# Kernel tuning notes

Hardware: AMD Instinct MI355X
Metric: run time of the kernel (lower is better)

Reference implementation:

```python
import jax, jax.numpy as jnp
import numpy as np

GROUPS = 32
NUM_HEADS = 8
EPS = 1e-5


def setup_inputs() -> dict:
    key = jax.random.key(0)
    ks = jax.random.split(key, 8)
    b, c, h, w = 2, 256, 64, 64
    x = jax.random.normal(ks[0], (b, c, h, w), dtype=jnp.float32)
    gn_w = jnp.ones((c,), dtype=jnp.float32)
    gn_b = jnp.zeros((c,), dtype=jnp.float32)
    qkv_w = jax.random.normal(ks[1], (3 * c, c), dtype=jnp.float32) * 0.02  # 1x1 conv
    qkv_b = jnp.zeros((3 * c,), dtype=jnp.float32)
    proj_w = jax.random.normal(ks[2], (c, c), dtype=jnp.float32) * 0.02  # 1x1 conv
    proj_b = jnp.zeros((c,), dtype=jnp.float32)
    return {"x": x, "gn_w": gn_w, "gn_b": gn_b, "qkv_w": qkv_w,
            "qkv_b": qkv_b, "proj_w": proj_w, "proj_b": proj_b}


def _group_norm(x, w, b):
    bsz, c, h, wd = x.shape
    xg = x.reshape(bsz, GROUPS, c // GROUPS, h * wd)
    mean = jnp.mean(xg, axis=(2, 3), keepdims=True)
    var = jnp.mean(jnp.square(xg - mean), axis=(2, 3), keepdims=True)
    xn = ((xg - mean) * jax.lax.rsqrt(var + EPS)).reshape(bsz, c, h, wd)
    return xn * w[None, :, None, None] + b[None, :, None, None]


def reference(x, gn_w, gn_b, qkv_w, qkv_b, proj_w, proj_b):
    b, c, h, w = x.shape
    hd = c // NUM_HEADS
    s = h * w
    xn = _group_norm(x, gn_w, gn_b)
    # 1x1 conv == channel matmul
    qkv = jnp.einsum('oc,bcs->bos', qkv_w, xn.reshape(b, c, s)) + qkv_b[None, :, None]
    qkv = qkv.reshape(b, 3, NUM_HEADS, hd, s)
    q, k, v = qkv[:, 0], qkv[:, 1], qkv[:, 2]  # (b, nh, hd, s)
    scale = 1.0 / jnp.sqrt(jnp.asarray(hd, dtype=x.dtype))
    scores = jnp.einsum('bhds,bhdt->bhst', q, k) * scale  # (b, nh, s, s)
    attn = jax.nn.softmax(scores, axis=-1)
    out = jnp.einsum('bhst,bhdt->bhds', attn, v)  # (b, nh, hd, s)
    out = out.reshape(b, c, h, w)
    out = jnp.einsum('oc,bcs->bos', proj_w, out.reshape(b, c, s)).reshape(b, c, h, w)
    out = out + proj_b[None, :, None, None]
    return out + x
```

## Files before the change

### kernel.cpp

```cpp
#include <hip/hip_runtime.h>
#include <hip/hip_bf16.h>

#define B_ 2
#define C_ 256
#define S_ 4096
#define NH 8
#define HD 32
#define EPSV 1e-5f
#define QSC2 0.25503487942324256f

typedef __bf16 bf16_t;
typedef bf16_t bf16x8 __attribute__((ext_vector_type(8)));
typedef float f32x4 __attribute__((ext_vector_type(4)));
typedef float f32x16 __attribute__((ext_vector_type(16)));
typedef int i32x2 __attribute__((ext_vector_type(2)));
typedef __hip_bfloat16 hbf;

__device__ inline unsigned cvtpk_bf16(float a, float b) {
  unsigned r;
  asm("v_cvt_pk_bf16_f32 %0, %1, %2" : "=v"(r) : "v"(a), "v"(b));
  return r;
}

#if __has_builtin(__builtin_amdgcn_exp2f)
#define EXP2R(x) __builtin_amdgcn_exp2f(x)
#else
#define EXP2R(x) exp2f(x)
#endif

__global__ __launch_bounds__(256) void f2bf_kernel(const float* __restrict__ src, hbf* __restrict__ dst, int n) {
  int i = blockIdx.x * 256 + threadIdx.x;
  if (i < n) dst[i] = __float2bfloat16(src[i]);
}

__global__ __launch_bounds__(256) void wfrag_kernel(const float* __restrict__ src, hbf* __restrict__ dst, int nchunks) {
  int i = blockIdx.x * 256 + threadIdx.x;
  if (i >= nchunks) return;
  int o = i >> 5, c8 = (i & 31) * 8;
  alignas(16) hbf tmp[8];
#pragma unroll
  for (int j = 0; j < 8; j++) tmp[j] = __float2bfloat16(src[(size_t)o * C_ + c8 + j]);
  *(uint4*)&dst[(((size_t)(o >> 5) * 16) + (c8 >> 4)) * 512 + (o & 31) * 16 + (c8 & 15)] = *(uint4*)tmp;
}

__global__ __launch_bounds__(1024) void gn_kernel(const float* __restrict__ x, const float* __restrict__ gw,
                                                  const float* __restrict__ gb, hbf* __restrict__ xn) {
  int b = blockIdx.x >> 5, g = blockIdx.x & 31;
  const float* xp = x + ((size_t)b * C_ + g * 8) * S_;
  float sum = 0.f, sumsq = 0.f;
  const float4* xp4 = (const float4*)xp;
  for (int i = threadIdx.x; i < 8 * S_ / 4; i += 1024) {
    float4 v = xp4[i];
    sum += v.x + v.y + v.z + v.w;
    sumsq += v.x * v.x + v.y * v.y + v.z * v.z + v.w * v.w;
  }
#pragma unroll
  for (int off = 32; off > 0; off >>= 1) {
    sum += __shfl_down(sum, off);
    sumsq += __shfl_down(sumsq, off);
  }
  __shared__ float red[2][16];
  int wid = threadIdx.x >> 6;
  if ((threadIdx.x & 63) == 0) { red[0][wid] = sum; red[1][wid] = sumsq; }
  __syncthreads();
  sum = 0.f; sumsq = 0.f;
#pragma unroll
  for (int k = 0; k < 16; k++) { sum += red[0][k]; sumsq += red[1][k]; }
  const float inv_n = 1.f / (8 * S_);
  float mean = sum * inv_n;
  float rstd = rsqrtf(fmaxf(sumsq * inv_n - mean * mean, 0.f) + EPSV);
  float scv[8], shv[8];
#pragma unroll
  for (int c = 0; c < 8; c++) {
    scv[c] = gw[g * 8 + c] * rstd;
    shv[c] = gb[g * 8 + c] - mean * scv[c];
  }
  for (int s = threadIdx.x; s < S_; s += 1024) {
    alignas(16) hbf tmp[8];
#pragma unroll
    for (int c = 0; c < 8; c++)
      tmp[c] = __float2bfloat16(xp[(size_t)c * S_ + s] * scv[c] + shv[c]);
    *(uint4*)&xn[(((size_t)b * (S_ >> 5) + (s >> 5)) * 16 + (g >> 1)) * 512 + (s & 31) * 16 + (g & 1) * 8] =
        *(uint4*)tmp;
  }
}

__global__ __launch_bounds__(512, 4) void qkv_gemm(const hbf* __restrict__ xn, const hbf* __restrict__ wf,
                                                   const float* __restrict__ bias,
                                                   hbf* __restrict__ qbuf, hbf* __restrict__ kg,
                                                   hbf* __restrict__ vg) {
  int bt = blockIdx.z;
  int m0 = blockIdx.x * 128;
  int n0 = blockIdx.y * 128;
  int tid = threadIdx.x, lane = tid & 63, w = tid >> 6;
  int wq = w & 3, wo = w >> 2;
  int l31 = lane & 31, hi = lane >> 5;
  const int loff = l31 * 16 + hi * 8;
  const hbf* ap = xn + ((size_t)bt * (S_ >> 5) + (m0 >> 5) + wq) * 8192;
  int oc0 = n0 + wo * 64;
  const hbf* bp0 = wf + (size_t)(oc0 >> 5) * 8192;
  const hbf* bp1 = bp0 + 8192;
  f32x16 acc0 = {0.f,0.f,0.f,0.f,0.f,0.f,0.f,0.f,0.f,0.f,0.f,0.f,0.f,0.f,0.f,0.f};
  f32x16 acc1 = acc0;
#pragma unroll 4
  for (int ks = 0; ks < 16; ++ks) {
    bf16x8 af = *(const bf16x8*)(ap + ks * 512 + loff);
    bf16x8 b0 = *(const bf16x8*)(bp0 + ks * 512 + loff);
    bf16x8 b1 = *(const bf16x8*)(bp1 + ks * 512 + loff);
    acc0 = __builtin_amdgcn_mfma_f32_32x32x16_bf16(af, b0, acc0, 0, 0, 0);
    acc1 = __builtin_amdgcn_mfma_f32_32x32x16_bf16(af, b1, acc1, 0, 0, 0);
  }
  int s_base = m0 + wq * 32;
#pragma unroll
  for (int ct = 0; ct < 2; ++ct) {
    f32x16 a = ct ? acc1 : acc0;
    int oc = oc0 + ct * 32;
    int o = oc + l31;
    float bs = bias[o];
    if (oc < 256) {
#pragma unroll
      for (int r = 0; r < 16; r++) {
        int s = s_base + (r & 3) + 8 * (r >> 2) + 4 * hi;
        qbuf[((size_t)bt * S_ + s) * C_ + o] = __float2bfloat16((a[r] + bs) * QSC2);
      }
    } else if (oc < 512) {
      int hh = (oc - 256) >> 5;
      const size_t khead = (size_t)(bt * NH + hh) * (S_ >> 5);
#pragma unroll
      for (int r = 0; r < 16; r++) {
        int s = s_base + (r & 3) + 8 * (r >> 2) + 4 * hi;
        kg[(khead + (s >> 5)) * 1024 + (l31 >> 4) * 512 + (s & 31) * 16 + (l31 & 15)] =
            __float2bfloat16(a[r] + bs);
      }
    } else {
      int hh = (oc - 512) >> 5;
      const size_t vhead = (size_t)(bt * NH + hh) * (S_ >> 4);
#pragma unroll
      for (int r = 0; r < 16; r++) {
        int s = s_base + (r & 3) + 8 * (r >> 2) + 4 * hi;
        vg[(vhead + (s >> 4)) * 512 + l31 * 16 + (s & 15)] = __float2bfloat16(a[r] + bs);
      }
    }
  }
}

__device__ inline void softmax_pv(f32x16 sc, bf16x8 va0, bf16x8 va1,
                                  f32x16& o_acc, float& l_run) {
#pragma unroll
  for (int i = 0; i < 16; i++) sc[i] = EXP2R(sc[i]);
  {
    float s0a = sc[0] + sc[1], s1a = sc[2] + sc[3], s2a = sc[4] + sc[5], s3a = sc[6] + sc[7];
    float s4a = sc[8] + sc[9], s5a = sc[10] + sc[11], s6a = sc[12] + sc[13], s7a = sc[14] + sc[15];
    s0a += s1a; s2a += s3a; s4a += s5a; s6a += s7a;
    s0a += s2a; s4a += s6a;
    l_run += s0a + s4a;
  }
#pragma unroll
  for (int kb = 0; kb < 2; kb++) {
    unsigned a0 = cvtpk_bf16(sc[kb * 8 + 0], sc[kb * 8 + 1]);
    unsigned b0 = cvtpk_bf16(sc[kb * 8 + 2], sc[kb * 8 + 3]);
    unsigned a1 = cvtpk_bf16(sc[kb * 8 + 4], sc[kb * 8 + 5]);
    unsigned b1 = cvtpk_bf16(sc[kb * 8 + 6], sc[kb * 8 + 7]);
    i32x2 ra = __builtin_amdgcn_permlane32_swap((int)a0, (int)a1, false, false);
    i32x2 rb = __builtin_amdgcn_permlane32_swap((int)b0, (int)b1, false, false);
    union { unsigned u[4]; bf16x8 v; } pf;
    pf.u[0] = (unsigned)ra[0]; pf.u[1] = (unsigned)rb[0];
    pf.u[2] = (unsigned)ra[1]; pf.u[3] = (unsigned)rb[1];
    o_acc = __builtin_amdgcn_mfma_f32_32x32x16_bf16(kb ? va1 : va0, pf.v, o_acc, 0, 0, 0);
  }
}

__global__ __launch_bounds__(512, 4) void attn_kernel(const hbf* __restrict__ qbuf, const hbf* __restrict__ kg,
                                                      const hbf* __restrict__ vg, hbf* __restrict__ attn_t) {
  int bid = blockIdx.x;
  int xcd = bid & 7, idx = bid >> 3;
  int combo = (xcd << 1) | (idx >> 6);
  int bt = combo >> 3, h = combo & 7;
  int s0 = (idx & 63) << 6;
  int tid = threadIdx.x, lane = tid & 63, w = tid >> 6;
  int wq = w & 1, wt = w >> 1;
  int l31 = lane & 31, hi = lane >> 5;
  const int loff = (l31 << 4) + (hi << 3);
  int qrow = s0 + wq * 32 + l31;
  bf16x8 qf0 = *(const bf16x8*)&qbuf[((size_t)bt * S_ + qrow) * C_ + h * HD + hi * 8];
  bf16x8 qf1 = *(const bf16x8*)&qbuf[((size_t)bt * S_ + qrow) * C_ + h * HD + 16 + hi * 8];
  f32x16 o_acc = {0.f,0.f,0.f,0.f,0.f,0.f,0.f,0.f,0.f,0.f,0.f,0.f,0.f,0.f,0.f,0.f};
  const f32x16 z16 = o_acc;
  float l_run = 0.f;
  const int tq0 = wt << 10;
  const hbf* kq = kg + ((size_t)(bt * NH + h) * (S_ >> 5) + (tq0 >> 5)) * 1024;
  const hbf* vq = vg + ((size_t)(bt * NH + h) * (S_ >> 4) + (tq0 >> 4)) * 512;
  bf16x8 ka0 = *(const bf16x8*)(kq + loff);
  bf16x8 ka1 = *(const bf16x8*)(kq + loff + 512);
  bf16x8 va0 = *(const bf16x8*)(vq + loff);
  bf16x8 va1 = *(const bf16x8*)(vq + loff + 512);
  f32x16 sc = __builtin_amdgcn_mfma_f32_32x32x16_bf16(ka0, qf0, z16, 0, 0, 0);
  sc = __builtin_amdgcn_mfma_f32_32x32x16_bf16(ka1, qf1, sc, 0, 0, 0);
  ka0 = *(const bf16x8*)(kq + 1024 + loff);
  ka1 = *(const bf16x8*)(kq + 1024 + loff + 512);
  kq += 2048;
  vq += 1024;
  for (int it = 1; it < 32; ++it) {
    bf16x8 kan0 = *(const bf16x8*)(kq + loff);
    bf16x8 kan1 = *(const bf16x8*)(kq + loff + 512);
    bf16x8 van0 = *(const bf16x8*)(vq + loff);
    bf16x8 van1 = *(const bf16x8*)(vq + loff + 512);
    f32x16 scn = __builtin_amdgcn_mfma_f32_32x32x16_bf16(ka0, qf0, z16, 0, 0, 0);
    scn = __builtin_amdgcn_mfma_f32_32x32x16_bf16(ka1, qf1, scn, 0, 0, 0);
    softmax_pv(sc, va0, va1, o_acc, l_run);
    sc = scn;
    ka0 = kan0; ka1 = kan1; va0 = van0; va1 = van1;
    kq += 1024; vq += 1024;
  }
  softmax_pv(sc, va0, va1, o_acc, l_run);
  __shared__ f32x16 ored[6 * 64];
  __shared__ float lred[8 * 64];
  __syncthreads();
  lred[(w << 6) + lane] = l_run;
  if (wt > 0) ored[((w - 2) << 6) + lane] = o_acc;
  __syncthreads();
  if (wt == 0) {
    float l_tot = 0.f;
#pragma unroll
    for (int k = 0; k < 4; k++) {
      int wp = wq + 2 * k;
      l_tot += lred[(wp << 6) + l31] + lred[(wp << 6) + 32 + l31];
    }
    f32x16 o = o_acc;
#pragma unroll
    for (int k = 0; k < 3; k++) {
      f32x16 t2 = ored[((wq + 2 * k) << 6) + lane];
#pragma unroll
      for (int i = 0; i < 16; i++) o[i] += t2[i];
    }
    float inv_l = 1.0f / l_tot;
#pragma unroll
    for (int c2 = 0; c2 < 4; c2++) {
      alignas(8) hbf tmp[4];
#pragma unroll
      for (int r = 0; r < 4; r++) tmp[r] = __float2bfloat16(o[c2 * 4 + r] * inv_l);
      *(uint2*)&attn_t[((size_t)bt * S_ + qrow) * C_ + h * HD + c2 * 8 + hi * 4] = *(uint2*)tmp;
    }
  }
}

__global__ __launch_bounds__(256) void proj_gemm(const hbf* __restrict__ attn_t, const hbf* __restrict__ wb,
                                                 const float* __restrict__ bias, const float* __restrict__ x,
                                                 float* __restrict__ out) {
  int bt = blockIdx.z;
  int m0 = blockIdx.x * 64;
  int n0 = blockIdx.y * 64;
  const hbf* A = attn_t + (size_t)bt * S_ * C_;
  __shared__ hbf a_lds[64][72];
  __shared__ hbf b_lds[64][72];
  int tid = threadIdx.x, lane = tid & 63, wid = tid >> 6;
  int wm = (wid >> 1) * 32, wn = (wid & 1) * 32;
  f32x4 acc[2][2] = {};
  for (int k0 = 0; k0 < C_; k0 += 64) {
    __syncthreads();
    int r = tid >> 3, kk = (tid & 7) * 8;
#pragma unroll
    for (int p = 0; p < 2; p++) {
      *(bf16x8*)&a_lds[r + p * 32][kk] = *(const bf16x8*)&A[(size_t)(m0 + r + p * 32) * C_ + k0 + kk];
      *(bf16x8*)&b_lds[r + p * 32][kk] = *(const bf16x8*)&wb[(size_t)(n0 + r + p * 32) * C_ + k0 + kk];
    }
    __syncthreads();
#pragma unroll
    for (int kk2 = 0; kk2 < 64; kk2 += 32) {
      bf16x8 af[2], bfr[2];
#pragma unroll
      for (int mi = 0; mi < 2; mi++)
        af[mi] = *(const bf16x8*)&a_lds[wm + mi * 16 + (lane & 15)][kk2 + (lane >> 4) * 8];
#pragma unroll
      for (int ni = 0; ni < 2; ni++)
        bfr[ni] = *(const bf16x8*)&b_lds[wn + ni * 16 + (lane & 15)][kk2 + (lane >> 4) * 8];
#pragma unroll
      for (int mi = 0; mi < 2; mi++)
#pragma unroll
        for (int ni = 0; ni < 2; ni++)
          acc[mi][ni] = __builtin_amdgcn_mfma_f32_16x16x32_bf16(af[mi], bfr[ni], acc[mi][ni], 0, 0, 0);
    }
  }
#pragma unroll
  for (int mi = 0; mi < 2; mi++)
#pragma unroll
    for (int ni = 0; ni < 2; ni++) {
      int o = n0 + wn + ni * 16 + (lane & 15);
      int s = m0 + wm + mi * 16 + (lane >> 4) * 4;
      size_t base = ((size_t)bt * C_ + o) * S_ + s;
      float pb = bias[o];
      float4 xr = *(const float4*)&x[base];
      float4 res;
      res.x = acc[mi][ni][0] + pb + xr.x;
      res.y = acc[mi][ni][1] + pb + xr.y;
      res.z = acc[mi][ni][2] + pb + xr.z;
      res.w = acc[mi][ni][3] + pb + xr.w;
      *(float4*)&out[base] = res;
    }
}

extern "C" void kernel_launch(void* const* d_in, const int* in_sizes, int n_in,
                              void* d_out, int out_size, void* d_ws, size_t ws_size,
                              hipStream_t stream) {
  const float* x = (const float*)d_in[0];
  const float* gn_w = (const float*)d_in[1];
  const float* gn_b = (const float*)d_in[2];
  const float* qkv_w = (const float*)d_in[3];
  const float* qkv_b = (const float*)d_in[4];
  const float* proj_w = (const float*)d_in[5];
  const float* proj_b = (const float*)d_in[6];
  float* out = (float*)d_out;

  hbf* qkv_wf = (hbf*)d_ws;
  hbf* proj_w_bf = qkv_wf + 768 * 256;
  hbf* xn = proj_w_bf + 256 * 256;
  hbf* qbuf = xn + (size_t)B_ * S_ * C_;
  hbf* kg = qbuf + (size_t)B_ * S_ * C_;
  hbf* vg = kg + (size_t)B_ * S_ * C_;
  hbf* attn_t = vg + (size_t)B_ * S_ * C_;

  dim3 blk(256);
  wfrag_kernel<<<(768 * 32 + 255) / 256, blk, 0, stream>>>(qkv_w, qkv_wf, 768 * 32);
  f2bf_kernel<<<(256 * 256 + 255) / 256, blk, 0, stream>>>(proj_w, proj_w_bf, 256 * 256);
  gn_kernel<<<64, dim3(1024), 0, stream>>>(x, gn_w, gn_b, xn);
  qkv_gemm<<<dim3(32, 6, 2), dim3(512), 0, stream>>>(xn, qkv_wf, qkv_b, qbuf, kg, vg);
  attn_kernel<<<dim3(1024), dim3(512), 0, stream>>>(qbuf, kg, vg, attn_t);
  proj_gemm<<<dim3(64, 4, 2), blk, 0, stream>>>(attn_t, proj_w_bf, proj_b, x, out);
}
```

Measured before the change: 85.43 us.

## Split group norm into stats and apply kernels; unroll attention loop by two

The single group-norm kernel, which ran only 64 blocks, becomes a two-pass scheme. A stats kernel of 512 blocks writes partial sums to workspace, and an apply kernel of 512 blocks reduces those partials and normalizes its own chunk. This spreads the memory-bound normalization across more CUs at the cost of one extra launch and a second read of x. The attention inner loop is also unrolled by two with interleaved K/V prefetches, which aims to give the scheduler more room to hide load latency behind MFMA and softmax work.

```diff
diff --git a/kernel.cpp b/kernel.cpp
--- a/kernel.cpp
+++ b/kernel.cpp
@@ -43,14 +43,15 @@
   *(uint4*)&dst[(((size_t)(o >> 5) * 16) + (c8 >> 4)) * 512 + (o & 31) * 16 + (c8 & 15)] = *(uint4*)tmp;
 }
 
-__global__ __launch_bounds__(1024) void gn_kernel(const float* __restrict__ x, const float* __restrict__ gw,
-                                                  const float* __restrict__ gb, hbf* __restrict__ xn) {
-  int b = blockIdx.x >> 5, g = blockIdx.x & 31;
-  const float* xp = x + ((size_t)b * C_ + g * 8) * S_;
+__global__ __launch_bounds__(256) void gn_stats(const float* __restrict__ x, float* __restrict__ stats) {
+  int bg = blockIdx.x >> 3, chunk = blockIdx.x & 7;
+  const float4* xp4 = (const float4*)(x + (size_t)bg * 8 * S_);
   float sum = 0.f, sumsq = 0.f;
-  const float4* xp4 = (const float4*)xp;
-  for (int i = threadIdx.x; i < 8 * S_ / 4; i += 1024) {
-    float4 v = xp4[i];
+#pragma unroll
+  for (int p = 0; p < 4; p++) {
+    int i = threadIdx.x + p * 256;
+    int ch = i >> 7, s4 = i & 127;
+    float4 v = xp4[ch * (S_ >> 2) + chunk * 128 + s4];
     sum += v.x + v.y + v.z + v.w;
     sumsq += v.x * v.x + v.y * v.y + v.z * v.z + v.w * v.w;
   }
@@ -59,13 +60,28 @@
     sum += __shfl_down(sum, off);
     sumsq += __shfl_down(sumsq, off);
   }
-  __shared__ float red[2][16];
+  __shared__ float red[2][4];
   int wid = threadIdx.x >> 6;
   if ((threadIdx.x & 63) == 0) { red[0][wid] = sum; red[1][wid] = sumsq; }
   __syncthreads();
-  sum = 0.f; sumsq = 0.f;
-#pragma unroll
-  for (int k = 0; k < 16; k++) { sum += red[0][k]; sumsq += red[1][k]; }
+  if (threadIdx.x == 0) {
+    stats[blockIdx.x * 2 + 0] = red[0][0] + red[0][1] + red[0][2] + red[0][3];
+    stats[blockIdx.x * 2 + 1] = red[1][0] + red[1][1] + red[1][2] + red[1][3];
+  }
+}
+
+__global__ __launch_bounds__(256) void gn_apply(const float* __restrict__ x, const float* __restrict__ gw,
+                                                const float* __restrict__ gb, const float* __restrict__ stats,
+                                                hbf* __restrict__ xn) {
+  int bg = blockIdx.x >> 3, chunk = blockIdx.x & 7;
+  int b = bg >> 5, g = bg & 31;
+  const float* xp = x + (size_t)bg * 8 * S_;
+  float sum = 0.f, sumsq = 0.f;
+#pragma unroll
+  for (int k = 0; k < 8; k++) {
+    sum += stats[(bg * 8 + k) * 2 + 0];
+    sumsq += stats[(bg * 8 + k) * 2 + 1];
+  }
   const float inv_n = 1.f / (8 * S_);
   float mean = sum * inv_n;
   float rstd = rsqrtf(fmaxf(sumsq * inv_n - mean * mean, 0.f) + EPSV);
@@ -75,7 +91,9 @@
     scv[c] = gw[g * 8 + c] * rstd;
     shv[c] = gb[g * 8 + c] - mean * scv[c];
   }
-  for (int s = threadIdx.x; s < S_; s += 1024) {
+#pragma unroll
+  for (int p = 0; p < 2; p++) {
+    int s = chunk * 512 + p * 256 + threadIdx.x;
     alignas(16) hbf tmp[8];
 #pragma unroll
     for (int c = 0; c < 8; c++)
@@ -190,29 +208,41 @@
   const int tq0 = wt << 10;
   const hbf* kq = kg + ((size_t)(bt * NH + h) * (S_ >> 5) + (tq0 >> 5)) * 1024;
   const hbf* vq = vg + ((size_t)(bt * NH + h) * (S_ >> 4) + (tq0 >> 4)) * 512;
-  bf16x8 ka0 = *(const bf16x8*)(kq + loff);
-  bf16x8 ka1 = *(const bf16x8*)(kq + loff + 512);
-  bf16x8 va0 = *(const bf16x8*)(vq + loff);
-  bf16x8 va1 = *(const bf16x8*)(vq + loff + 512);
-  f32x16 sc = __builtin_amdgcn_mfma_f32_32x32x16_bf16(ka0, qf0, z16, 0, 0, 0);
-  sc = __builtin_amdgcn_mfma_f32_32x32x16_bf16(ka1, qf1, sc, 0, 0, 0);
-  ka0 = *(const bf16x8*)(kq + 1024 + loff);
-  ka1 = *(const bf16x8*)(kq + 1024 + loff + 512);
+  bf16x8 kaB0 = *(const bf16x8*)(kq + loff);
+  bf16x8 kaB1 = *(const bf16x8*)(kq + loff + 512);
+  f32x16 scA = __builtin_amdgcn_mfma_f32_32x32x16_bf16(kaB0, qf0, z16, 0, 0, 0);
+  scA = __builtin_amdgcn_mfma_f32_32x32x16_bf16(kaB1, qf1, scA, 0, 0, 0);
+  kaB0 = *(const bf16x8*)(kq + loff + 1024);
+  kaB1 = *(const bf16x8*)(kq + loff + 1536);
+  bf16x8 vaA0 = *(const bf16x8*)(vq + loff);
+  bf16x8 vaA1 = *(const bf16x8*)(vq + loff + 512);
   kq += 2048;
   vq += 1024;
-  for (int it = 1; it < 32; ++it) {
-    bf16x8 kan0 = *(const bf16x8*)(kq + loff);
-    bf16x8 kan1 = *(const bf16x8*)(kq + loff + 512);
-    bf16x8 van0 = *(const bf16x8*)(vq + loff);
-    bf16x8 van1 = *(const bf16x8*)(vq + loff + 512);
-    f32x16 scn = __builtin_amdgcn_mfma_f32_32x32x16_bf16(ka0, qf0, z16, 0, 0, 0);
-    scn = __builtin_amdgcn_mfma_f32_32x32x16_bf16(ka1, qf1, scn, 0, 0, 0);
-    softmax_pv(sc, va0, va1, o_acc, l_run);
-    sc = scn;
-    ka0 = kan0; ka1 = kan1; va0 = van0; va1 = van1;
-    kq += 1024; vq += 1024;
-  }
-  softmax_pv(sc, va0, va1, o_acc, l_run);
+  for (int j = 0; j < 15; ++j) {
+    bf16x8 vaB0 = *(const bf16x8*)(vq + loff);
+    bf16x8 vaB1 = *(const bf16x8*)(vq + loff + 512);
+    bf16x8 knA0 = *(const bf16x8*)(kq + loff);
+    bf16x8 knA1 = *(const bf16x8*)(kq + loff + 512);
+    f32x16 scB = __builtin_amdgcn_mfma_f32_32x32x16_bf16(kaB0, qf0, z16, 0, 0, 0);
+    scB = __builtin_amdgcn_mfma_f32_32x32x16_bf16(kaB1, qf1, scB, 0, 0, 0);
+    kaB0 = *(const bf16x8*)(kq + loff + 1024);
+    kaB1 = *(const bf16x8*)(kq + loff + 1536);
+    softmax_pv(scA, vaA0, vaA1, o_acc, l_run);
+    vaA0 = *(const bf16x8*)(vq + loff + 1024);
+    vaA1 = *(const bf16x8*)(vq + loff + 1536);
+    scA = __builtin_amdgcn_mfma_f32_32x32x16_bf16(knA0, qf0, z16, 0, 0, 0);
+    scA = __builtin_amdgcn_mfma_f32_32x32x16_bf16(knA1, qf1, scA, 0, 0, 0);
+    softmax_pv(scB, vaB0, vaB1, o_acc, l_run);
+    kq += 2048; vq += 2048;
+  }
+  {
+    bf16x8 vaB0 = *(const bf16x8*)(vq + loff);
+    bf16x8 vaB1 = *(const bf16x8*)(vq + loff + 512);
+    f32x16 scB = __builtin_amdgcn_mfma_f32_32x32x16_bf16(kaB0, qf0, z16, 0, 0, 0);
+    scB = __builtin_amdgcn_mfma_f32_32x32x16_bf16(kaB1, qf1, scB, 0, 0, 0);
+    softmax_pv(scA, vaA0, vaA1, o_acc, l_run);
+    softmax_pv(scB, vaB0, vaB1, o_acc, l_run);
+  }
   __shared__ f32x16 ored[6 * 64];
   __shared__ float lred[8 * 64];
   __syncthreads();
@@ -318,11 +348,13 @@
   hbf* kg = qbuf + (size_t)B_ * S_ * C_;
   hbf* vg = kg + (size_t)B_ * S_ * C_;
   hbf* attn_t = vg + (size_t)B_ * S_ * C_;
+  float* stats = (float*)(attn_t + (size_t)B_ * S_ * C_);
 
   dim3 blk(256);
   wfrag_kernel<<<(768 * 32 + 255) / 256, blk, 0, stream>>>(qkv_w, qkv_wf, 768 * 32);
   f2bf_kernel<<<(256 * 256 + 255) / 256, blk, 0, stream>>>(proj_w, proj_w_bf, 256 * 256);
-  gn_kernel<<<64, dim3(1024), 0, stream>>>(x, gn_w, gn_b, xn);
+  gn_stats<<<512, blk, 0, stream>>>(x, stats);
+  gn_apply<<<512, blk, 0, stream>>>(x, gn_w, gn_b, stats, xn);
   qkv_gemm<<<dim3(32, 6, 2), dim3(512), 0, stream>>>(xn, qkv_wf, qkv_b, qbuf, kg, vg);
   attn_kernel<<<dim3(1024), dim3(512), 0, stream>>>(qbuf, kg, vg, attn_t);
   proj_gemm<<<dim3(64, 4, 2), blk, 0, stream>>>(attn_t, proj_w_bf, proj_b, x, out);
```

New measurement: 83.28 us. 1.03x faster.
